# Optimization experiments

Measured on AMD Instinct MI355X. Metric: run time of the kernel, lower is better.

## Reference

```python
import jax, jax.numpy as jnp
import numpy as np
from jax import lax

KERNEL = 3
STRIDE = 1
PADDING = 1
DILATION = 1


def setup_inputs() -> dict:
    key = jax.random.key(0)
    k1, k2, k3, k4, k5 = jax.random.split(key, 5)
    B, C, H, W = 8, 64, 256, 256
    x = jax.random.normal(k1, (B, C, H, W), dtype=jnp.float32)
    depthwise_weights = jax.random.normal(k2, (C, 1, KERNEL, KERNEL), dtype=jnp.float32)
    pointwise_weights = jax.random.normal(k3, (C, C, 1, 1), dtype=jnp.float32)
    attention_weights = jax.random.normal(k4, (C, C), dtype=jnp.float32)
    global_attention_weight = jax.random.normal(k5, (C, C), dtype=jnp.float32)
    return {
        "x": x,
        "depthwise_weights": depthwise_weights,
        "pointwise_weights": pointwise_weights,
        "attention_weights": attention_weights,
        "global_attention_weight": global_attention_weight,
    }


def reference(x, depthwise_weights, pointwise_weights, attention_weights, global_attention_weight):
    C = x.shape[1]
    # Depthwise conv: groups == C, NCHW / OIHW layout.
    dw = lax.conv_general_dilated(
        x,
        depthwise_weights,
        window_strides=(STRIDE, STRIDE),
        padding=[(PADDING, PADDING), (PADDING, PADDING)],
        rhs_dilation=(DILATION, DILATION),
        feature_group_count=C,
        dimension_numbers=("NCHW", "OIHW", "NCHW"),
    )  # [B, C, Ho, Wo]
    # Per-pixel channel attention (row-softmax over mixing matrix).
    A = jax.nn.softmax(attention_weights, axis=1)  # [C, C]
    att = jnp.einsum("cd,bdhw->bchw", A, dw)
    # 1x1 pointwise conv (channel mix).
    pw = jnp.einsum("kc,bchw->bkhw", pointwise_weights[:, :, 0, 0], att)
    # Global channel attention.
    G = jax.nn.softmax(global_attention_weight, axis=1)  # [C, C]
    out = jnp.einsum("cd,bdhw->bchw", G, pw)
    return out
```

## Files before the change

### kernel.cpp

```cpp
#include <hip/hip_runtime.h>
#include <math.h>

#define HH 256
#define WW 256
#define CC 64
#define NB 8

__global__ __launch_bounds__(1024) void prep_M(const float* __restrict__ A,
                                               const float* __restrict__ G,
                                               const float* __restrict__ P,
                                               float* __restrict__ Mt) {
    __shared__ __align__(16) float As[64][68];
    __shared__ __align__(16) float Gs[64][68];
    __shared__ __align__(16) float T[64][68];

    const int t = threadIdx.x;
    const int wave = t >> 6;
    const int lane = t & 63;

    for (int r8 = 0; r8 < 8; ++r8) {
        int row = wave * 8 + r8;
        int r = row & 63;
        const float* src = (row < 64) ? A : G;
        float v = src[r * 64 + lane];
        float m = v;
        #pragma unroll
        for (int off = 32; off > 0; off >>= 1)
            m = fmaxf(m, __shfl_xor(m, off, 64));
        float e = __expf(v - m);
        float s = e;
        #pragma unroll
        for (int off = 32; off > 0; off >>= 1)
            s += __shfl_xor(s, off, 64);
        float o = e / s;
        if (row < 64) As[r][lane] = o; else Gs[r][lane] = o;
    }
    __syncthreads();

    {
        const int d = t >> 4, q = t & 15;
        float4 acc = make_float4(0.f, 0.f, 0.f, 0.f);
        for (int e = 0; e < 64; ++e) {
            float p = P[d * 64 + e];
            float4 a = *(const float4*)&As[e][4 * q];
            acc.x = fmaf(p, a.x, acc.x);
            acc.y = fmaf(p, a.y, acc.y);
            acc.z = fmaf(p, a.z, acc.z);
            acc.w = fmaf(p, a.w, acc.w);
        }
        *(float4*)&T[d][4 * q] = acc;
    }
    __syncthreads();

    {
        const int k = t >> 4, q = t & 15;
        float4 acc = make_float4(0.f, 0.f, 0.f, 0.f);
        for (int d = 0; d < 64; ++d) {
            float g = Gs[k][d];
            float4 tv = *(const float4*)&T[d][4 * q];
            acc.x = fmaf(g, tv.x, acc.x);
            acc.y = fmaf(g, tv.y, acc.y);
            acc.z = fmaf(g, tv.z, acc.z);
            acc.w = fmaf(g, tv.w, acc.w);
        }
        Mt[(4 * q + 0) * 64 + k] = acc.x;
        Mt[(4 * q + 1) * 64 + k] = acc.y;
        Mt[(4 * q + 2) * 64 + k] = acc.z;
        Mt[(4 * q + 3) * 64 + k] = acc.w;
    }
}

__global__ __launch_bounds__(256) void fused_conv_mix(const float* __restrict__ x,
                                                      const float* __restrict__ dwgt,
                                                      const float* __restrict__ Mt,
                                                      float* __restrict__ out) {
    __shared__ __align__(16) float MtS[64][68];
    __shared__ __align__(16) float dwS[64][68];

    const int t = threadIdx.x;
    const int tw0 = blockIdx.x * 64;
    const int h = blockIdx.y;
    const int b = blockIdx.z;

    {
        #pragma unroll
        for (int j = 0; j < 4; ++j) {
            int idx = (j * 256 + t) * 4;
            int row = idx >> 6;
            int col = idx & 63;
            float4 v = *(const float4*)(Mt + idx);
            *(float4*)&MtS[row][col] = v;
        }
    }

    {
        const int c = t >> 2;
        const int chunk = t & 3;
        const int gw0 = tw0 + chunk * 16;
        const float* xc = x + ((size_t)(b * CC + c) * HH) * WW;

        float r[3][18];
        #pragma unroll
        for (int dy = 0; dy < 3; ++dy) {
            int y = h + dy - 1;
            if ((unsigned)y < (unsigned)HH) {
                const float* p = xc + y * WW + gw0;
                const float4* p4 = (const float4*)p;
                float4 v0 = p4[0], v1 = p4[1], v2 = p4[2], v3 = p4[3];
                r[dy][1] = v0.x;  r[dy][2] = v0.y;  r[dy][3] = v0.z;  r[dy][4] = v0.w;
                r[dy][5] = v1.x;  r[dy][6] = v1.y;  r[dy][7] = v1.z;  r[dy][8] = v1.w;
                r[dy][9] = v2.x;  r[dy][10] = v2.y; r[dy][11] = v2.z; r[dy][12] = v2.w;
                r[dy][13] = v3.x; r[dy][14] = v3.y; r[dy][15] = v3.z; r[dy][16] = v3.w;
                r[dy][0]  = (gw0 > 0)        ? p[-1] : 0.f;
                r[dy][17] = (gw0 + 16 < WW)  ? p[16] : 0.f;
            } else {
                #pragma unroll
                for (int i = 0; i < 18; ++i) r[dy][i] = 0.f;
            }
        }

        float wg[9];
        #pragma unroll
        for (int i = 0; i < 9; ++i) wg[i] = dwgt[c * 9 + i];

        float acc[16];
        #pragma unroll
        for (int i = 0; i < 16; ++i) {
            float a = 0.f;
            #pragma unroll
            for (int dy = 0; dy < 3; ++dy)
                #pragma unroll
                for (int dx = 0; dx < 3; ++dx)
                    a = fmaf(wg[dy * 3 + dx], r[dy][i + dx], a);
            acc[i] = a;
        }

        #pragma unroll
        for (int v = 0; v < 4; ++v) {
            float4 w4 = make_float4(acc[4 * v + 0], acc[4 * v + 1],
                                    acc[4 * v + 2], acc[4 * v + 3]);
            *(float4*)&dwS[c][chunk * 16 + 4 * v] = w4;
        }
    }

    __syncthreads();

    {
        const int ki = t >> 4;
        const int wj = t & 15;
        float o00 = 0.f, o01 = 0.f, o02 = 0.f, o03 = 0.f;
        float o10 = 0.f, o11 = 0.f, o12 = 0.f, o13 = 0.f;
        float o20 = 0.f, o21 = 0.f, o22 = 0.f, o23 = 0.f;
        float o30 = 0.f, o31 = 0.f, o32 = 0.f, o33 = 0.f;

        #pragma unroll 4
        for (int c = 0; c < 64; ++c) {
            float4 m = *(const float4*)&MtS[c][4 * ki];
            float4 d = *(const float4*)&dwS[c][4 * wj];
            o00 = fmaf(m.x, d.x, o00); o01 = fmaf(m.x, d.y, o01);
            o02 = fmaf(m.x, d.z, o02); o03 = fmaf(m.x, d.w, o03);
            o10 = fmaf(m.y, d.x, o10); o11 = fmaf(m.y, d.y, o11);
            o12 = fmaf(m.y, d.z, o12); o13 = fmaf(m.y, d.w, o13);
            o20 = fmaf(m.z, d.x, o20); o21 = fmaf(m.z, d.y, o21);
            o22 = fmaf(m.z, d.z, o22); o23 = fmaf(m.z, d.w, o23);
            o30 = fmaf(m.w, d.x, o30); o31 = fmaf(m.w, d.y, o31);
            o32 = fmaf(m.w, d.z, o32); o33 = fmaf(m.w, d.w, o33);
        }

        float* ob = out + ((size_t)(b * CC) * HH + h) * WW + tw0 + 4 * wj;
        const size_t kstride = (size_t)HH * WW;
        {
            int k = 4 * ki;
            *(float4*)(ob + (size_t)(k + 0) * kstride) = make_float4(o00, o01, o02, o03);
            *(float4*)(ob + (size_t)(k + 1) * kstride) = make_float4(o10, o11, o12, o13);
            *(float4*)(ob + (size_t)(k + 2) * kstride) = make_float4(o20, o21, o22, o23);
            *(float4*)(ob + (size_t)(k + 3) * kstride) = make_float4(o30, o31, o32, o33);
        }
    }
}

extern "C" void kernel_launch(void* const* d_in, const int* in_sizes, int n_in,
                              void* d_out, int out_size, void* d_ws, size_t ws_size,
                              hipStream_t stream) {
    const float* x    = (const float*)d_in[0];
    const float* dwgt = (const float*)d_in[1];
    const float* pwgt = (const float*)d_in[2];
    const float* attw = (const float*)d_in[3];
    const float* gatt = (const float*)d_in[4];
    float* Mt = (float*)d_ws;
    float* o  = (float*)d_out;

    prep_M<<<1, 1024, 0, stream>>>(attw, gatt, pwgt, Mt);

    dim3 grid(WW / 64, HH, NB);
    fused_conv_mix<<<grid, 256, 0, stream>>>(x, dwgt, Mt, o);
}
```

Before: 299.5 us.

## Process eight rows per block with rolling row registers and double-buffered LDS

Each block now covers eight output rows instead of one. The three input rows for the depthwise stencil are kept in registers and rotated, so each x row is read roughly once rather than three times, and the Mt load into LDS is amortized across rows. A double-buffered dwS lets the next row's load overlap the channel-mix GEMM, and outputs are written with nontemporal stores. In exchange the grid has eight times fewer blocks and register pressure rises (launch bounds set to 3 blocks), which could reduce occupancy.

```diff
diff --git a/kernel.cpp b/kernel.cpp
--- a/kernel.cpp
+++ b/kernel.cpp
@@ -5,6 +5,9 @@
 #define WW 256
 #define CC 64
 #define NB 8
+#define ROWS 8
+
+typedef float fvec4 __attribute__((ext_vector_type(4)));
 
 __global__ __launch_bounds__(1024) void prep_M(const float* __restrict__ A,
                                                const float* __restrict__ G,
@@ -70,112 +73,123 @@
     }
 }
 
-__global__ __launch_bounds__(256) void fused_conv_mix(const float* __restrict__ x,
-                                                      const float* __restrict__ dwgt,
-                                                      const float* __restrict__ Mt,
-                                                      float* __restrict__ out) {
-    __shared__ __align__(16) float MtS[64][68];
-    __shared__ __align__(16) float dwS[64][68];
+__global__ __launch_bounds__(256, 3) void fused_conv_mix(const float* __restrict__ x,
+                                                         const float* __restrict__ dwgt,
+                                                         const float* __restrict__ Mt,
+                                                         float* __restrict__ out) {
+    __shared__ __align__(16) float MtS[64][64];
+    __shared__ __align__(16) float dwS[2][64][68];
 
     const int t = threadIdx.x;
     const int tw0 = blockIdx.x * 64;
-    const int h = blockIdx.y;
+    const int h0 = blockIdx.y * ROWS;
     const int b = blockIdx.z;
 
     {
-        #pragma unroll
-        for (int j = 0; j < 4; ++j) {
-            int idx = (j * 256 + t) * 4;
-            int row = idx >> 6;
-            int col = idx & 63;
-            float4 v = *(const float4*)(Mt + idx);
-            *(float4*)&MtS[row][col] = v;
-        }
-    }
-
-    {
-        const int c = t >> 2;
-        const int chunk = t & 3;
-        const int gw0 = tw0 + chunk * 16;
-        const float* xc = x + ((size_t)(b * CC + c) * HH) * WW;
-
-        float r[3][18];
-        #pragma unroll
-        for (int dy = 0; dy < 3; ++dy) {
-            int y = h + dy - 1;
-            if ((unsigned)y < (unsigned)HH) {
-                const float* p = xc + y * WW + gw0;
-                const float4* p4 = (const float4*)p;
-                float4 v0 = p4[0], v1 = p4[1], v2 = p4[2], v3 = p4[3];
-                r[dy][1] = v0.x;  r[dy][2] = v0.y;  r[dy][3] = v0.z;  r[dy][4] = v0.w;
-                r[dy][5] = v1.x;  r[dy][6] = v1.y;  r[dy][7] = v1.z;  r[dy][8] = v1.w;
-                r[dy][9] = v2.x;  r[dy][10] = v2.y; r[dy][11] = v2.z; r[dy][12] = v2.w;
-                r[dy][13] = v3.x; r[dy][14] = v3.y; r[dy][15] = v3.z; r[dy][16] = v3.w;
-                r[dy][0]  = (gw0 > 0)        ? p[-1] : 0.f;
-                r[dy][17] = (gw0 + 16 < WW)  ? p[16] : 0.f;
-            } else {
+        const float4* m4 = (const float4*)Mt;
+        float4* s4 = (float4*)&MtS[0][0];
+        #pragma unroll
+        for (int j = 0; j < 4; ++j) s4[j * 256 + t] = m4[j * 256 + t];
+    }
+
+    const int c = t >> 2;
+    const int chunk = t & 3;
+    const int gw0 = tw0 + chunk * 16;
+    const float* xc = x + ((size_t)(b * CC + c) * HH) * WW;
+
+    float wg[9];
+    #pragma unroll
+    for (int i = 0; i < 9; ++i) wg[i] = dwgt[c * 9 + i];
+
+    float rm[18], r0[18], rp[18], rn[18];
+
+    auto load_row = [&](float* r, int y) {
+        if ((unsigned)y < (unsigned)HH) {
+            const float* p = xc + y * WW + gw0;
+            const float4* p4 = (const float4*)p;
+            float4 v0 = p4[0], v1 = p4[1], v2 = p4[2], v3 = p4[3];
+            r[1] = v0.x;  r[2] = v0.y;  r[3] = v0.z;  r[4] = v0.w;
+            r[5] = v1.x;  r[6] = v1.y;  r[7] = v1.z;  r[8] = v1.w;
+            r[9] = v2.x;  r[10] = v2.y; r[11] = v2.z; r[12] = v2.w;
+            r[13] = v3.x; r[14] = v3.y; r[15] = v3.z; r[16] = v3.w;
+            r[0]  = (gw0 > 0)       ? p[-1] : 0.f;
+            r[17] = (gw0 + 16 < WW) ? p[16] : 0.f;
+        } else {
+            #pragma unroll
+            for (int i = 0; i < 18; ++i) r[i] = 0.f;
+        }
+    };
+
+    load_row(rm, h0 - 1);
+    load_row(r0, h0);
+    load_row(rp, h0 + 1);
+
+    __syncthreads();
+
+    const int ki = t >> 4;
+    const int wj = t & 15;
+    const size_t kstride = (size_t)HH * WW;
+
+    #pragma unroll 1
+    for (int i = 0; i < ROWS; ++i) {
+        {
+            #pragma unroll
+            for (int v = 0; v < 4; ++v) {
+                float4 o4;
+                float* oo = (float*)&o4;
                 #pragma unroll
-                for (int i = 0; i < 18; ++i) r[dy][i] = 0.f;
+                for (int u = 0; u < 4; ++u) {
+                    int j = 4 * v + u;
+                    float a = 0.f;
+                    #pragma unroll
+                    for (int dx = 0; dx < 3; ++dx) {
+                        a = fmaf(wg[0 * 3 + dx], rm[j + dx], a);
+                        a = fmaf(wg[1 * 3 + dx], r0[j + dx], a);
+                        a = fmaf(wg[2 * 3 + dx], rp[j + dx], a);
+                    }
+                    oo[u] = a;
+                }
+                *(float4*)&dwS[i & 1][c][chunk * 16 + 4 * v] = o4;
             }
         }
-
-        float wg[9];
-        #pragma unroll
-        for (int i = 0; i < 9; ++i) wg[i] = dwgt[c * 9 + i];
-
-        float acc[16];
-        #pragma unroll
-        for (int i = 0; i < 16; ++i) {
-            float a = 0.f;
-            #pragma unroll
-            for (int dy = 0; dy < 3; ++dy)
-                #pragma unroll
-                for (int dx = 0; dx < 3; ++dx)
-                    a = fmaf(wg[dy * 3 + dx], r[dy][i + dx], a);
-            acc[i] = a;
-        }
-
-        #pragma unroll
-        for (int v = 0; v < 4; ++v) {
-            float4 w4 = make_float4(acc[4 * v + 0], acc[4 * v + 1],
-                                    acc[4 * v + 2], acc[4 * v + 3]);
-            *(float4*)&dwS[c][chunk * 16 + 4 * v] = w4;
-        }
-    }
-
-    __syncthreads();
-
-    {
-        const int ki = t >> 4;
-        const int wj = t & 15;
-        float o00 = 0.f, o01 = 0.f, o02 = 0.f, o03 = 0.f;
-        float o10 = 0.f, o11 = 0.f, o12 = 0.f, o13 = 0.f;
-        float o20 = 0.f, o21 = 0.f, o22 = 0.f, o23 = 0.f;
-        float o30 = 0.f, o31 = 0.f, o32 = 0.f, o33 = 0.f;
-
-        #pragma unroll 4
-        for (int c = 0; c < 64; ++c) {
-            float4 m = *(const float4*)&MtS[c][4 * ki];
-            float4 d = *(const float4*)&dwS[c][4 * wj];
-            o00 = fmaf(m.x, d.x, o00); o01 = fmaf(m.x, d.y, o01);
-            o02 = fmaf(m.x, d.z, o02); o03 = fmaf(m.x, d.w, o03);
-            o10 = fmaf(m.y, d.x, o10); o11 = fmaf(m.y, d.y, o11);
-            o12 = fmaf(m.y, d.z, o12); o13 = fmaf(m.y, d.w, o13);
-            o20 = fmaf(m.z, d.x, o20); o21 = fmaf(m.z, d.y, o21);
-            o22 = fmaf(m.z, d.z, o22); o23 = fmaf(m.z, d.w, o23);
-            o30 = fmaf(m.w, d.x, o30); o31 = fmaf(m.w, d.y, o31);
-            o32 = fmaf(m.w, d.z, o32); o33 = fmaf(m.w, d.w, o33);
-        }
-
-        float* ob = out + ((size_t)(b * CC) * HH + h) * WW + tw0 + 4 * wj;
-        const size_t kstride = (size_t)HH * WW;
+        __syncthreads();
+
+        if (i < ROWS - 1) load_row(rn, h0 + i + 2);
+
         {
-            int k = 4 * ki;
-            *(float4*)(ob + (size_t)(k + 0) * kstride) = make_float4(o00, o01, o02, o03);
-            *(float4*)(ob + (size_t)(k + 1) * kstride) = make_float4(o10, o11, o12, o13);
-            *(float4*)(ob + (size_t)(k + 2) * kstride) = make_float4(o20, o21, o22, o23);
-            *(float4*)(ob + (size_t)(k + 3) * kstride) = make_float4(o30, o31, o32, o33);
-        }
+            float o00 = 0.f, o01 = 0.f, o02 = 0.f, o03 = 0.f;
+            float o10 = 0.f, o11 = 0.f, o12 = 0.f, o13 = 0.f;
+            float o20 = 0.f, o21 = 0.f, o22 = 0.f, o23 = 0.f;
+            float o30 = 0.f, o31 = 0.f, o32 = 0.f, o33 = 0.f;
+
+            #pragma unroll 4
+            for (int cc2 = 0; cc2 < 64; ++cc2) {
+                float4 m = *(const float4*)&MtS[cc2][4 * ki];
+                float4 d = *(const float4*)&dwS[i & 1][cc2][4 * wj];
+                o00 = fmaf(m.x, d.x, o00); o01 = fmaf(m.x, d.y, o01);
+                o02 = fmaf(m.x, d.z, o02); o03 = fmaf(m.x, d.w, o03);
+                o10 = fmaf(m.y, d.x, o10); o11 = fmaf(m.y, d.y, o11);
+                o12 = fmaf(m.y, d.z, o12); o13 = fmaf(m.y, d.w, o13);
+                o20 = fmaf(m.z, d.x, o20); o21 = fmaf(m.z, d.y, o21);
+                o22 = fmaf(m.z, d.z, o22); o23 = fmaf(m.z, d.w, o23);
+                o30 = fmaf(m.w, d.x, o30); o31 = fmaf(m.w, d.y, o31);
+                o32 = fmaf(m.w, d.z, o32); o33 = fmaf(m.w, d.w, o33);
+            }
+
+            float* ob = out + ((size_t)(b * CC) * HH + (h0 + i)) * WW + tw0 + 4 * wj;
+            const int k = 4 * ki;
+            fvec4 s0 = {o00, o01, o02, o03};
+            fvec4 s1 = {o10, o11, o12, o13};
+            fvec4 s2 = {o20, o21, o22, o23};
+            fvec4 s3 = {o30, o31, o32, o33};
+            __builtin_nontemporal_store(s0, (fvec4*)(ob + (size_t)(k + 0) * kstride));
+            __builtin_nontemporal_store(s1, (fvec4*)(ob + (size_t)(k + 1) * kstride));
+            __builtin_nontemporal_store(s2, (fvec4*)(ob + (size_t)(k + 2) * kstride));
+            __builtin_nontemporal_store(s3, (fvec4*)(ob + (size_t)(k + 3) * kstride));
+        }
+
+        #pragma unroll
+        for (int j = 0; j < 18; ++j) { rm[j] = r0[j]; r0[j] = rp[j]; rp[j] = rn[j]; }
     }
 }
 
@@ -192,6 +206,6 @@
 
     prep_M<<<1, 1024, 0, stream>>>(attw, gatt, pwgt, Mt);
 
-    dim3 grid(WW / 64, HH, NB);
+    dim3 grid(WW / 64, HH / ROWS, NB);
     fused_conv_mix<<<grid, 256, 0, stream>>>(x, dwgt, Mt, o);
 }
```

Result: faster. 287.2 us (-4.1%).
